# Optimization experiments

Hardware: AMD Instinct MI355X
Metric: run time of the kernel (lower is better)

Reference implementation:

```python
import jax, jax.numpy as jnp
import numpy as np

N_NODES = 100000
N_EDGES = 800000
D_IN = 128
D_HID = 128
D_OUT = 128
NUM_GRAPHS = 64


def gcn_conv(x, src, dst, W, b, n_nodes):
    """PyG GCNConv: h = D^{-1/2} (A + I) D^{-1/2} (x W) + b, with self-loops included in src/dst."""
    h = x @ W  # [N, d_out]
    deg = jax.ops.segment_sum(jnp.ones_like(dst, dtype=h.dtype), dst, num_segments=n_nodes)
    dinv = jnp.where(deg > 0, jax.lax.rsqrt(deg), 0.0)
    norm = dinv[src] * dinv[dst]  # [E]
    out = jax.ops.segment_sum(h[src] * norm[:, None], dst, num_segments=n_nodes)
    return out + b


def setup_inputs() -> dict:
    key = jax.random.key(0)
    ks = jax.random.split(key, 10)
    x = jax.random.normal(ks[0], (N_NODES, D_IN), dtype=jnp.float32)
    edge_index = jax.random.randint(ks[1], (2, N_EDGES), 0, N_NODES, dtype=jnp.int64)
    batch = jnp.sort(jax.random.randint(ks[2], (N_NODES,), 0, NUM_GRAPHS, dtype=jnp.int64))
    s1 = 1.0 / np.sqrt(D_IN)
    s2 = 1.0 / np.sqrt(D_HID)
    W1 = jax.random.uniform(ks[3], (D_IN, D_HID), jnp.float32, -s1, s1)
    b1 = jnp.zeros((D_HID,), jnp.float32)
    W2 = jax.random.uniform(ks[4], (D_HID, D_HID), jnp.float32, -s2, s2)
    b2 = jnp.zeros((D_HID,), jnp.float32)
    Wfc = jax.random.uniform(ks[5], (D_HID, D_OUT), jnp.float32, -s2, s2)
    bfc = jax.random.uniform(ks[6], (D_OUT,), jnp.float32, -s2, s2)
    return {"x": x, "edge_index": edge_index, "batch": batch,
            "W1": W1, "b1": b1, "W2": W2, "b2": b2, "Wfc": Wfc, "bfc": bfc}


def reference(x, edge_index, batch, W1, b1, W2, b2, Wfc, bfc):
    n = x.shape[0]
    loop = jnp.arange(n, dtype=edge_index.dtype)
    src = jnp.concatenate([edge_index[0], loop])
    dst = jnp.concatenate([edge_index[1], loop])
    h = jax.nn.relu(gcn_conv(x, src, dst, W1, b1, n))
    h = jax.nn.relu(gcn_conv(h, src, dst, W2, b2, n))
    # global_mean_pool over graph ids
    sums = jax.ops.segment_sum(h, batch, num_segments=NUM_GRAPHS)
    cnts = jax.ops.segment_sum(jnp.ones((n,), h.dtype), batch, num_segments=NUM_GRAPHS)
    pooled = sums / jnp.maximum(cnts, 1.0)[:, None]
    return pooled @ Wfc + bfc
```

## Files before the change

### kernel.cpp

```cpp
#include <hip/hip_runtime.h>
#include <hip/hip_bf16.h>

#define N_NODES 100000
#define N_EDGES 800000
#define D 128
#define NG 64
#define SCAN_NB ((N_NODES + 255) / 256)
#define NTILES ((N_NODES + 63) / 64)

typedef __attribute__((ext_vector_type(8))) short short8;
typedef __attribute__((ext_vector_type(4))) float f32x4;

static __device__ __forceinline__ unsigned short f2bf(float f) {
    unsigned u = __float_as_uint(f);
    unsigned r = (u + 0x7FFF + ((u >> 16) & 1)) >> 16;
    return (unsigned short)r;
}
static __device__ __forceinline__ float bf2f(unsigned short b) {
    return __uint_as_float((unsigned)b << 16);
}


__global__ void hist_kernel(const int* __restrict__ dst, int* __restrict__ deg) {
    int e = blockIdx.x * blockDim.x + threadIdx.x;
    if (e < N_EDGES) atomicAdd(&deg[dst[e]], 1);
}

__global__ void dinv_kernel(const int* __restrict__ deg, float* __restrict__ dinv) {
    int i = blockIdx.x * blockDim.x + threadIdx.x;
    if (i < N_NODES) dinv[i] = rsqrtf((float)deg[i] + 1.0f);
}

__global__ __launch_bounds__(256) void scan1_kernel(const int* __restrict__ deg,
                                                    int* __restrict__ rs,
                                                    int* __restrict__ bsum) {
    __shared__ int wsum[4];
    int i = blockIdx.x * 256 + threadIdx.x;
    int lane = threadIdx.x & 63;
    int wid = threadIdx.x >> 6;
    int v = (i < N_NODES) ? deg[i] : 0;
    int x = v;
    #pragma unroll
    for (int off = 1; off < 64; off <<= 1) {
        int y = __shfl_up(x, off);
        if (lane >= off) x += y;
    }
    if (lane == 63) wsum[wid] = x;
    __syncthreads();
    int add = 0;
    #pragma unroll
    for (int w = 0; w < 3; ++w) if (w < wid) add += wsum[w];
    int incl = x + add;
    if (i < N_NODES) rs[i] = incl - v;
    if (threadIdx.x == 255) bsum[blockIdx.x] = incl;
}

__global__ __launch_bounds__(512) void scan2_kernel(int* __restrict__ bsum) {
    __shared__ int s[512];
    int t = threadIdx.x;
    int v = (t < SCAN_NB) ? bsum[t] : 0;
    s[t] = v;
    __syncthreads();
    for (int off = 1; off < 512; off <<= 1) {
        int y = (t >= off) ? s[t - off] : 0;
        __syncthreads();
        s[t] += y;
        __syncthreads();
    }
    if (t < SCAN_NB) bsum[t] = s[t] - v;
}

__global__ void scan3_kernel(int* __restrict__ rs, const int* __restrict__ bsum) {
    int i = blockIdx.x * blockDim.x + threadIdx.x;
    if (i < N_NODES) rs[i] += bsum[i >> 8];
    if (i == 0) rs[N_NODES] = N_EDGES;
}

__global__ void fill_kernel(const int* __restrict__ src, const int* __restrict__ dst,
                            const float* __restrict__ dinv, const int* __restrict__ rs,
                            int* __restrict__ cursor, int2* __restrict__ pairs) {
    int e = blockIdx.x * blockDim.x + threadIdx.x;
    if (e < N_EDGES) {
        int d = dst[e];
        int s = src[e];
        int p = rs[d] + atomicAdd(&cursor[d], 1);
        pairs[p] = make_int2(s, __float_as_int(dinv[s] * dinv[d]));
    }
}


__global__ void bounds_kernel(const int* __restrict__ batch, int* __restrict__ start) {
    int g = threadIdx.x;
    if (g > NG) return;
    if (g == NG) { start[NG] = N_NODES; return; }
    int lo = 0, hi = N_NODES;
    while (lo < hi) {
        int mid = (lo + hi) >> 1;
        if (batch[mid] < g) lo = mid + 1; else hi = mid;
    }
    start[g] = lo;
}


template <bool IN_F32>
__global__ __launch_bounds__(512) void xw_mfma_kernel(const void* __restrict__ Xin,
                                                      const float* __restrict__ W,
                                                      unsigned short* __restrict__ Hout) {
    __shared__ __align__(16) unsigned short bt_hi[128 * 128];
    __shared__ __align__(16) unsigned short bt_lo[128 * 128];
    __shared__ __align__(16) unsigned short atile[64 * 128];

    const int t = threadIdx.x;
    const int lane = t & 63;
    const int wid = t >> 6;

    #pragma unroll 4
    for (int i = 0; i < 32; ++i) {
        int idx = t + i * 512;
        int k = idx >> 7;
        int n = idx & 127;
        float w = W[idx];
        unsigned short hi = f2bf(w);
        unsigned short lo = f2bf(w - bf2f(hi));
        int byte = (n * 256 + k * 2) ^ ((n & 7) << 4);
        *(unsigned short*)((char*)bt_hi + byte) = hi;
        *(unsigned short*)((char*)bt_lo + byte) = lo;
    }

    const int mrow = (wid >> 1) * 16;
    const int ncol = (wid & 1) * 64;
    const int ar = mrow + (lane & 15);
    const int ak = (lane >> 4) * 8;

    for (int tile = blockIdx.x; tile < NTILES; tile += gridDim.x) {
        const int node0 = tile * 64;
        __syncthreads();

        #pragma unroll
        for (int p = 0; p < 2; ++p) {
            int j = t + p * 512;
            int row = j >> 4;
            int c8 = (j & 15) * 8;
            int node = node0 + row;
            short8 v = 0;
            if (IN_F32) {
                const float* X = (const float*)Xin;
                if (node < N_NODES) {
                    const float* xr = &X[(size_t)node * 128 + c8];
                    float4 a = *(const float4*)xr;
                    float4 b = *(const float4*)(xr + 4);
                    v[0] = (short)f2bf(a.x); v[1] = (short)f2bf(a.y);
                    v[2] = (short)f2bf(a.z); v[3] = (short)f2bf(a.w);
                    v[4] = (short)f2bf(b.x); v[5] = (short)f2bf(b.y);
                    v[6] = (short)f2bf(b.z); v[7] = (short)f2bf(b.w);
                }
            } else {
                const unsigned short* X = (const unsigned short*)Xin;
                if (node < N_NODES) v = *(const short8*)&X[(size_t)node * 128 + c8];
            }
            int byte = (row * 256 + c8 * 2) ^ ((row & 7) << 4);
            *(short8*)((char*)atile + byte) = v;
        }
        __syncthreads();

        f32x4 acc[4];
        #pragma unroll
        for (int nt = 0; nt < 4; ++nt) acc[nt] = 0.f;

        #pragma unroll
        for (int kc = 0; kc < 128; kc += 32) {
            short8 a = *(const short8*)((const char*)atile +
                        ((ar * 256 + (kc + ak) * 2) ^ ((ar & 7) << 4)));
            #pragma unroll
            for (int nt = 0; nt < 4; ++nt) {
                int col = ncol + nt * 16 + (lane & 15);
                int boff = (col * 256 + (kc + ak) * 2) ^ ((col & 7) << 4);
                short8 bh = *(const short8*)((const char*)bt_hi + boff);
                acc[nt] = __builtin_amdgcn_mfma_f32_16x16x32_bf16(a, bh, acc[nt], 0, 0, 0);
                short8 bl = *(const short8*)((const char*)bt_lo + boff);
                acc[nt] = __builtin_amdgcn_mfma_f32_16x16x32_bf16(a, bl, acc[nt], 0, 0, 0);
            }
        }

        #pragma unroll
        for (int nt = 0; nt < 4; ++nt) {
            #pragma unroll
            for (int r = 0; r < 4; ++r) {
                int node = node0 + mrow + (lane >> 4) * 4 + r;
                if (node < N_NODES)
                    Hout[(size_t)node * 128 + ncol + nt * 16 + (lane & 15)] = f2bf(acc[nt][r]);
            }
        }
    }
}


__global__ __launch_bounds__(256) void gather_kernel(const unsigned short* __restrict__ H,
                                                     const int* __restrict__ rs,
                                                     const int2* __restrict__ pairs,
                                                     const float* __restrict__ dinv,
                                                     const float* __restrict__ bias,
                                                     unsigned short* __restrict__ out) {
    int node = blockIdx.x * 4 + (threadIdx.x >> 6);
    if (node >= N_NODES) return;
    int lane = threadIdx.x & 63;

    float di = dinv[node];
    ushort2 hv = *(const ushort2*)&H[(size_t)node * 128 + lane * 2];
    float2 bb = *(const float2*)&bias[lane * 2];
    float ax = bf2f(hv.x) * di * di + bb.x;
    float ay = bf2f(hv.y) * di * di + bb.y;

    int beg = rs[node];
    int end = rs[node + 1];
    int i = beg;
    for (; i + 3 < end; i += 4) {
        int2 p0 = pairs[i];
        int2 p1 = pairs[i + 1];
        int2 p2 = pairs[i + 2];
        int2 p3 = pairs[i + 3];
        ushort2 h0 = *(const ushort2*)&H[(size_t)p0.x * 128 + lane * 2];
        ushort2 h1 = *(const ushort2*)&H[(size_t)p1.x * 128 + lane * 2];
        ushort2 h2 = *(const ushort2*)&H[(size_t)p2.x * 128 + lane * 2];
        ushort2 h3 = *(const ushort2*)&H[(size_t)p3.x * 128 + lane * 2];
        float w0 = __int_as_float(p0.y), w1 = __int_as_float(p1.y);
        float w2 = __int_as_float(p2.y), w3 = __int_as_float(p3.y);
        ax = fmaf(bf2f(h0.x), w0, ax); ay = fmaf(bf2f(h0.y), w0, ay);
        ax = fmaf(bf2f(h1.x), w1, ax); ay = fmaf(bf2f(h1.y), w1, ay);
        ax = fmaf(bf2f(h2.x), w2, ax); ay = fmaf(bf2f(h2.y), w2, ay);
        ax = fmaf(bf2f(h3.x), w3, ax); ay = fmaf(bf2f(h3.y), w3, ay);
    }
    for (; i < end; ++i) {
        int2 p = pairs[i];
        float w = __int_as_float(p.y);
        ushort2 h = *(const ushort2*)&H[(size_t)p.x * 128 + lane * 2];
        ax = fmaf(bf2f(h.x), w, ax);
        ay = fmaf(bf2f(h.y), w, ay);
    }
    ushort2 o;
    o.x = f2bf(fmaxf(ax, 0.f));
    o.y = f2bf(fmaxf(ay, 0.f));
    *(ushort2*)&out[(size_t)node * 128 + lane * 2] = o;
}


__global__ __launch_bounds__(256) void pool_kernel(const unsigned short* __restrict__ H,
                                                   const int* __restrict__ start,
                                                   float* __restrict__ sums) {
    __shared__ float red[16][132];
    int g = blockIdx.x >> 4;
    int s = blockIdx.x & 15;
    int n0 = start[g], n1 = start[g + 1];
    int slot = threadIdx.x & 15;
    int nl = threadIdx.x >> 4;

    float acc[8];
    #pragma unroll
    for (int j = 0; j < 8; ++j) acc[j] = 0.f;

    for (int node = n0 + s * 16 + nl; node < n1; node += 256) {
        short8 v = *(const short8*)&H[(size_t)node * 128 + slot * 8];
        #pragma unroll
        for (int j = 0; j < 8; ++j) acc[j] += bf2f((unsigned short)v[j]);
    }

    #pragma unroll
    for (int j = 0; j < 8; ++j) red[nl][slot * 8 + j] = acc[j];
    __syncthreads();
    #pragma unroll
    for (int off = 8; off > 0; off >>= 1) {
        if (nl < off) {
            #pragma unroll
            for (int j = 0; j < 8; ++j)
                red[nl][slot * 8 + j] += red[nl + off][slot * 8 + j];
        }
        __syncthreads();
    }
    if (nl == 0) {
        #pragma unroll
        for (int j = 0; j < 8; ++j)
            unsafeAtomicAdd(&sums[g * D + slot * 8 + j], red[0][slot * 8 + j]);
    }
}


__global__ void fc_kernel(const float* __restrict__ sums, const int* __restrict__ start,
                          const float* __restrict__ Wfc, const float* __restrict__ bfc,
                          float* __restrict__ out) {
    __shared__ __align__(16) float ps[D];
    int g = blockIdx.x;
    int f = threadIdx.x;
    float c = (float)max(start[g + 1] - start[g], 1);
    ps[f] = sums[g * D + f] / c;
    __syncthreads();
    float acc = bfc[f];
    #pragma unroll
    for (int k = 0; k < D; k += 4) {
        float4 pv = *(const float4*)&ps[k];
        acc += pv.x * Wfc[k * D + f] + pv.y * Wfc[(k + 1) * D + f] +
               pv.z * Wfc[(k + 2) * D + f] + pv.w * Wfc[(k + 3) * D + f];
    }
    out[g * D + f] = acc;
}

extern "C" void kernel_launch(void* const* d_in, const int* in_sizes, int n_in,
                              void* d_out, int out_size, void* d_ws, size_t ws_size,
                              hipStream_t stream) {
    const float* x   = (const float*)d_in[0];
    const int* ei    = (const int*)d_in[1];
    const int* batch = (const int*)d_in[2];
    const float* W1  = (const float*)d_in[3];
    const float* b1  = (const float*)d_in[4];
    const float* W2  = (const float*)d_in[5];
    const float* b2  = (const float*)d_in[6];
    const float* Wfc = (const float*)d_in[7];
    const float* bfc = (const float*)d_in[8];
    float* out = (float*)d_out;

    const int* src = ei;
    const int* dst = ei + N_EDGES;

    int2* pairs          = (int2*)d_ws;
    unsigned short* H1   = (unsigned short*)(pairs + N_EDGES);
    unsigned short* H2   = H1 + (size_t)N_NODES * D;
    float* dinv          = (float*)(H2 + (size_t)N_NODES * D);
    int*   deg           = (int*)(dinv + N_NODES);
    int*   rs            = deg + N_NODES;
    int*   cursor        = rs + N_NODES + 4;
    int*   bsum          = cursor + N_NODES;
    int*   start         = bsum + 512;
    float* sums          = (float*)(start + NG + 8);

    hipMemsetAsync(deg, 0, N_NODES * sizeof(int), stream);
    hipMemsetAsync(cursor, 0, N_NODES * sizeof(int), stream);
    hipMemsetAsync(sums, 0, NG * D * sizeof(float), stream);

    hist_kernel<<<(N_EDGES + 255) / 256, 256, 0, stream>>>(dst, deg);
    dinv_kernel<<<(N_NODES + 255) / 256, 256, 0, stream>>>(deg, dinv);
    scan1_kernel<<<SCAN_NB, 256, 0, stream>>>(deg, rs, bsum);
    scan2_kernel<<<1, 512, 0, stream>>>(bsum);
    scan3_kernel<<<SCAN_NB, 256, 0, stream>>>(rs, bsum);
    fill_kernel<<<(N_EDGES + 255) / 256, 256, 0, stream>>>(src, dst, dinv, rs, cursor, pairs);
    bounds_kernel<<<1, 128, 0, stream>>>(batch, start);

    xw_mfma_kernel<true><<<512, 512, 0, stream>>>(x, W1, H1);
    gather_kernel<<<(N_NODES + 3) / 4, 256, 0, stream>>>(H1, rs, pairs, dinv, b1, H2);

    xw_mfma_kernel<false><<<512, 512, 0, stream>>>(H2, W2, H1);
    gather_kernel<<<(N_NODES + 3) / 4, 256, 0, stream>>>(H1, rs, pairs, dinv, b2, H2);

    pool_kernel<<<NG * 16, 256, 0, stream>>>(H2, start, sums);
    fc_kernel<<<NG, 128, 0, stream>>>(sums, start, Wfc, bfc, out);
}
```

Baseline: 336.5 us.

## Store XW output in FP8 and unroll gather by eight with clamped indices

The dense transform now writes its output as FP8 (e4m3) instead of bf16, which halves the bytes the edge-gather kernel has to read for each neighbour row. The gather loop becomes a fixed 8-wide unrolled loop that clamps indices and zeroes the weights of padded slots, to keep more loads in flight. The dinv computation is folded into scan1 and the two memsets are merged, removing one launch and one memset. FP8 storage loses substantial precision in the hidden features and may put the output outside tolerance.

```diff
diff --git a/kernel.cpp b/kernel.cpp
--- a/kernel.cpp
+++ b/kernel.cpp
@@ -10,6 +10,7 @@
 
 typedef __attribute__((ext_vector_type(8))) short short8;
 typedef __attribute__((ext_vector_type(4))) float f32x4;
+typedef __attribute__((ext_vector_type(2))) float f32x2;
 
 static __device__ __forceinline__ unsigned short f2bf(float f) {
     unsigned u = __float_as_uint(f);
@@ -19,6 +20,13 @@
 static __device__ __forceinline__ float bf2f(unsigned short b) {
     return __uint_as_float((unsigned)b << 16);
 }
+static __device__ __forceinline__ unsigned char f2fp8(float v) {
+    int p = __builtin_amdgcn_cvt_pk_fp8_f32(v, v, 0, false);
+    return (unsigned char)(p & 0xFF);
+}
+static __device__ __forceinline__ f32x2 fp8x2_f32(unsigned short s) {
+    return __builtin_amdgcn_cvt_pk_f32_fp8((int)s, false);
+}
 
 
 __global__ void hist_kernel(const int* __restrict__ dst, int* __restrict__ deg) {
@@ -26,19 +34,16 @@
     if (e < N_EDGES) atomicAdd(&deg[dst[e]], 1);
 }
 
-__global__ void dinv_kernel(const int* __restrict__ deg, float* __restrict__ dinv) {
-    int i = blockIdx.x * blockDim.x + threadIdx.x;
-    if (i < N_NODES) dinv[i] = rsqrtf((float)deg[i] + 1.0f);
-}
-
 __global__ __launch_bounds__(256) void scan1_kernel(const int* __restrict__ deg,
                                                     int* __restrict__ rs,
-                                                    int* __restrict__ bsum) {
+                                                    int* __restrict__ bsum,
+                                                    float* __restrict__ dinv) {
     __shared__ int wsum[4];
     int i = blockIdx.x * 256 + threadIdx.x;
     int lane = threadIdx.x & 63;
     int wid = threadIdx.x >> 6;
     int v = (i < N_NODES) ? deg[i] : 0;
+    if (i < N_NODES) dinv[i] = rsqrtf((float)v + 1.0f);
     int x = v;
     #pragma unroll
     for (int off = 1; off < 64; off <<= 1) {
@@ -105,7 +110,7 @@
 template <bool IN_F32>
 __global__ __launch_bounds__(512) void xw_mfma_kernel(const void* __restrict__ Xin,
                                                       const float* __restrict__ W,
-                                                      unsigned short* __restrict__ Hout) {
+                                                      unsigned char* __restrict__ Hq) {
     __shared__ __align__(16) unsigned short bt_hi[128 * 128];
     __shared__ __align__(16) unsigned short bt_lo[128 * 128];
     __shared__ __align__(16) unsigned short atile[64 * 128];
@@ -188,14 +193,14 @@
             for (int r = 0; r < 4; ++r) {
                 int node = node0 + mrow + (lane >> 4) * 4 + r;
                 if (node < N_NODES)
-                    Hout[(size_t)node * 128 + ncol + nt * 16 + (lane & 15)] = f2bf(acc[nt][r]);
+                    Hq[(size_t)node * 128 + ncol + nt * 16 + (lane & 15)] = f2fp8(acc[nt][r]);
             }
         }
     }
 }
 
 
-__global__ __launch_bounds__(256) void gather_kernel(const unsigned short* __restrict__ H,
+__global__ __launch_bounds__(256) void gather_kernel(const unsigned char* __restrict__ Hq,
                                                      const int* __restrict__ rs,
                                                      const int2* __restrict__ pairs,
                                                      const float* __restrict__ dinv,
@@ -206,36 +211,28 @@
     int lane = threadIdx.x & 63;
 
     float di = dinv[node];
-    ushort2 hv = *(const ushort2*)&H[(size_t)node * 128 + lane * 2];
+    unsigned short sv = *(const unsigned short*)&Hq[(size_t)node * 128 + lane * 2];
+    f32x2 hs = fp8x2_f32(sv);
     float2 bb = *(const float2*)&bias[lane * 2];
-    float ax = bf2f(hv.x) * di * di + bb.x;
-    float ay = bf2f(hv.y) * di * di + bb.y;
+    float ax = hs[0] * di * di + bb.x;
+    float ay = hs[1] * di * di + bb.y;
 
     int beg = rs[node];
     int end = rs[node + 1];
-    int i = beg;
-    for (; i + 3 < end; i += 4) {
-        int2 p0 = pairs[i];
-        int2 p1 = pairs[i + 1];
-        int2 p2 = pairs[i + 2];
-        int2 p3 = pairs[i + 3];
-        ushort2 h0 = *(const ushort2*)&H[(size_t)p0.x * 128 + lane * 2];
-        ushort2 h1 = *(const ushort2*)&H[(size_t)p1.x * 128 + lane * 2];
-        ushort2 h2 = *(const ushort2*)&H[(size_t)p2.x * 128 + lane * 2];
-        ushort2 h3 = *(const ushort2*)&H[(size_t)p3.x * 128 + lane * 2];
-        float w0 = __int_as_float(p0.y), w1 = __int_as_float(p1.y);
-        float w2 = __int_as_float(p2.y), w3 = __int_as_float(p3.y);
-        ax = fmaf(bf2f(h0.x), w0, ax); ay = fmaf(bf2f(h0.y), w0, ay);
-        ax = fmaf(bf2f(h1.x), w1, ax); ay = fmaf(bf2f(h1.y), w1, ay);
-        ax = fmaf(bf2f(h2.x), w2, ax); ay = fmaf(bf2f(h2.y), w2, ay);
-        ax = fmaf(bf2f(h3.x), w3, ax); ay = fmaf(bf2f(h3.y), w3, ay);
-    }
-    for (; i < end; ++i) {
-        int2 p = pairs[i];
-        float w = __int_as_float(p.y);
-        ushort2 h = *(const ushort2*)&H[(size_t)p.x * 128 + lane * 2];
-        ax = fmaf(bf2f(h.x), w, ax);
-        ay = fmaf(bf2f(h.y), w, ay);
+    if (end > beg) {
+        int last = end - 1;
+        for (int i = beg; i < end; i += 8) {
+            #pragma unroll
+            for (int j = 0; j < 8; ++j) {
+                int idx = i + j;
+                int2 p = pairs[min(idx, last)];
+                float w = (idx < end) ? __int_as_float(p.y) : 0.f;
+                unsigned short hv = *(const unsigned short*)&Hq[(size_t)p.x * 128 + lane * 2];
+                f32x2 hf = fp8x2_f32(hv);
+                ax = fmaf(hf[0], w, ax);
+                ay = fmaf(hf[1], w, ay);
+            }
+        }
     }
     ushort2 o;
     o.x = f2bf(fmaxf(ax, 0.f));
@@ -244,7 +241,7 @@
 }
 
 
-__global__ __launch_bounds__(256) void pool_kernel(const unsigned short* __restrict__ H,
+__global__ __launch_bounds__(256) void pool_kernel(const unsigned short* __restrict__ G,
                                                    const int* __restrict__ start,
                                                    float* __restrict__ sums) {
     __shared__ float red[16][132];
@@ -259,7 +256,7 @@
     for (int j = 0; j < 8; ++j) acc[j] = 0.f;
 
     for (int node = n0 + s * 16 + nl; node < n1; node += 256) {
-        short8 v = *(const short8*)&H[(size_t)node * 128 + slot * 8];
+        short8 v = *(const short8*)&G[(size_t)node * 128 + slot * 8];
         #pragma unroll
         for (int j = 0; j < 8; ++j) acc[j] += bf2f((unsigned short)v[j]);
     }
@@ -320,35 +317,33 @@
     const int* src = ei;
     const int* dst = ei + N_EDGES;
 
-    int2* pairs          = (int2*)d_ws;
-    unsigned short* H1   = (unsigned short*)(pairs + N_EDGES);
-    unsigned short* H2   = H1 + (size_t)N_NODES * D;
-    float* dinv          = (float*)(H2 + (size_t)N_NODES * D);
+    unsigned char* Hq    = (unsigned char*)d_ws;
+    unsigned short* G    = (unsigned short*)(Hq + (size_t)N_NODES * D);
+    int2* pairs          = (int2*)(G + (size_t)N_NODES * D);
+    float* dinv          = (float*)(pairs + N_EDGES);
     int*   deg           = (int*)(dinv + N_NODES);
-    int*   rs            = deg + N_NODES;
-    int*   cursor        = rs + N_NODES + 4;
-    int*   bsum          = cursor + N_NODES;
+    int*   cursor        = deg + N_NODES;
+    int*   rs            = cursor + N_NODES;
+    int*   bsum          = rs + N_NODES + 4;
     int*   start         = bsum + 512;
     float* sums          = (float*)(start + NG + 8);
 
-    hipMemsetAsync(deg, 0, N_NODES * sizeof(int), stream);
-    hipMemsetAsync(cursor, 0, N_NODES * sizeof(int), stream);
+    hipMemsetAsync(deg, 0, 2 * N_NODES * sizeof(int), stream);
     hipMemsetAsync(sums, 0, NG * D * sizeof(float), stream);
 
     hist_kernel<<<(N_EDGES + 255) / 256, 256, 0, stream>>>(dst, deg);
-    dinv_kernel<<<(N_NODES + 255) / 256, 256, 0, stream>>>(deg, dinv);
-    scan1_kernel<<<SCAN_NB, 256, 0, stream>>>(deg, rs, bsum);
+    scan1_kernel<<<SCAN_NB, 256, 0, stream>>>(deg, rs, bsum, dinv);
     scan2_kernel<<<1, 512, 0, stream>>>(bsum);
     scan3_kernel<<<SCAN_NB, 256, 0, stream>>>(rs, bsum);
     fill_kernel<<<(N_EDGES + 255) / 256, 256, 0, stream>>>(src, dst, dinv, rs, cursor, pairs);
     bounds_kernel<<<1, 128, 0, stream>>>(batch, start);
 
-    xw_mfma_kernel<true><<<512, 512, 0, stream>>>(x, W1, H1);
-    gather_kernel<<<(N_NODES + 3) / 4, 256, 0, stream>>>(H1, rs, pairs, dinv, b1, H2);
-
-    xw_mfma_kernel<false><<<512, 512, 0, stream>>>(H2, W2, H1);
-    gather_kernel<<<(N_NODES + 3) / 4, 256, 0, stream>>>(H1, rs, pairs, dinv, b2, H2);
-
-    pool_kernel<<<NG * 16, 256, 0, stream>>>(H2, start, sums);
+    xw_mfma_kernel<true><<<512, 512, 0, stream>>>(x, W1, Hq);
+    gather_kernel<<<(N_NODES + 3) / 4, 256, 0, stream>>>(Hq, rs, pairs, dinv, b1, G);
+
+    xw_mfma_kernel<false><<<512, 512, 0, stream>>>(G, W2, Hq);
+    gather_kernel<<<(N_NODES + 3) / 4, 256, 0, stream>>>(Hq, rs, pairs, dinv, b2, G);
+
+    pool_kernel<<<NG * 16, 256, 0, stream>>>(G, start, sums);
     fc_kernel<<<NG, 128, 0, stream>>>(sums, start, Wfc, bfc, out);
 }
```

After: 374.9 us. 1.11x slower.
